# Optimization experiments

Hardware: AMD Instinct MI355X
Metric: run time of the kernel (lower is better)

The kernel has to match this reference:

```python
import jax, jax.numpy as jnp
import numpy as np

H, W, C, B = 64, 64, 512, 16

def _dwconv(x, w, b, k):
    # x: [B,C,H,W]; w: [C,1,k,k] depthwise kernel; b: [C]
    pad = k // 2
    out = jax.lax.conv_general_dilated(
        x, w, window_strides=(1, 1), padding=[(pad, pad), (pad, pad)],
        dimension_numbers=('NCHW', 'OIHW', 'NCHW'), feature_group_count=x.shape[1])
    return out + b[None, :, None, None]

def setup_inputs() -> dict:
    key = jax.random.key(0)
    ks = jax.random.split(key, 7)
    x = jax.random.normal(ks[0], (B, 1 + H * W, C), dtype=jnp.float32)
    def kinit(k, ksize):
        fan_in = ksize * ksize  # groups=C -> in_ch per group = 1
        bound = 1.0 / np.sqrt(fan_in)
        return jax.random.uniform(k, (C, 1, ksize, ksize), jnp.float32, -bound, bound)
    w7 = kinit(ks[1], 7); b7 = jax.random.uniform(ks[2], (C,), jnp.float32, -1/7.0, 1/7.0)
    w5 = kinit(ks[3], 5); b5 = jax.random.uniform(ks[4], (C,), jnp.float32, -1/5.0, 1/5.0)
    w3 = kinit(ks[5], 3); b3 = jax.random.uniform(ks[6], (C,), jnp.float32, -1/3.0, 1/3.0)
    return {'x': x, 'w7': w7, 'b7': b7, 'w5': w5, 'b5': b5, 'w3': w3, 'b3': b3}

def reference(x, w7, b7, w5, b5, w3, b3):
    Bn, N, Cn = x.shape
    cls_token = x[:, 0]          # [B, C]
    feat_token = x[:, 1:]        # [B, H*W, C]
    cnn_feat = feat_token.transpose(0, 2, 1).reshape(Bn, Cn, H, W)
    y = (_dwconv(cnn_feat, w7, b7, 7) + cnn_feat
         + _dwconv(cnn_feat, w5, b5, 5)
         + _dwconv(cnn_feat, w3, b3, 3))
    y = y.reshape(Bn, Cn, H * W).transpose(0, 2, 1)   # [B, HW, C]
    return jnp.concatenate([cls_token[:, None, :], y], axis=1)
```

## Files before the change

kernel.cpp:

```cpp
#include <hip/hip_runtime.h>

#define Hh 64
#define Ww 64
#define Cc 512
#define Bb 16
#define NTOK (1 + Hh * Ww)
#define TW 8
#define TH 2

__global__ void ppeg_prep(const float* __restrict__ w7, const float* __restrict__ b7,
                          const float* __restrict__ w5, const float* __restrict__ b5,
                          const float* __restrict__ w3, const float* __restrict__ b3,
                          const float* __restrict__ x, float* __restrict__ wt,
                          float* __restrict__ beff, float* __restrict__ out) {
    int idx = blockIdx.x * blockDim.x + threadIdx.x;
    if (idx < Cc * 49) {
        int c = idx / 49, t = idx % 49;
        int r = t / 7, s = t % 7;
        float v = w7[idx];
        if (r >= 1 && r <= 5 && s >= 1 && s <= 5) v += w5[c * 25 + (r - 1) * 5 + (s - 1)];
        if (r >= 2 && r <= 4 && s >= 2 && s <= 4) v += w3[c * 9 + (r - 2) * 3 + (s - 2)];
        if (t == 24) v += 1.0f;
        wt[t * Cc + c] = v;
    }
    if (idx < Cc) beff[idx] = b7[idx] + b5[idx] + b3[idx];
    if (idx < Bb * Cc) {
        int b = idx / Cc, c = idx % Cc;
        size_t o = (size_t)b * NTOK * Cc + c;
        out[o] = x[o];
    }
}

__global__ __launch_bounds__(256)
void ppeg_conv(const float* __restrict__ x, const float* __restrict__ wt,
               const float* __restrict__ beff, float* __restrict__ out) {
    const int tx = threadIdx.x;
    const int ty = threadIdx.y;
    const int cb = blockIdx.y * 64;
    const int c  = cb + tx;
    const int b  = blockIdx.z;
    const int sp = blockIdx.x;
    const int hblk  = sp >> 3;
    const int wblk  = sp & 7;
    const int oh0   = hblk * (TH * 4) + ty * TH;
    const int wbase = wblk * TW;

    const float* xb = x + ((size_t)b * NTOK + 1) * Cc + c;

    const float bias = beff[c];
    float acc[TH][TW];
#pragma unroll
    for (int o = 0; o < TH; ++o)
#pragma unroll
        for (int j = 0; j < TW; ++j) acc[o][j] = bias;

    const bool interior = (wblk != 0) && (wblk != 7);

#pragma unroll
    for (int r = 0; r < 7; ++r) {
        float tap[7];
#pragma unroll
        for (int s = 0; s < 7; ++s) tap[s] = wt[(r * 7 + s) * Cc + c];

#pragma unroll
        for (int o = 0; o < TH; ++o) {
            const int ir = oh0 + o + r - 3;
            if (ir < 0 || ir >= Hh) continue;
            const float* xrow = xb + (size_t)ir * Ww * Cc;
            float v[TW + 6];
            if (interior) {
#pragma unroll
                for (int j = 0; j < TW + 6; ++j)
                    v[j] = xrow[(size_t)(wbase - 3 + j) * Cc];
            } else {
#pragma unroll
                for (int j = 0; j < TW + 6; ++j) {
                    const int wc = wbase + j - 3;
                    v[j] = (wc >= 0 && wc < Ww) ? xrow[(size_t)wc * Cc] : 0.0f;
                }
            }
#pragma unroll
            for (int j = 0; j < TW; ++j)
#pragma unroll
                for (int s = 0; s < 7; ++s)
                    acc[o][j] = fmaf(tap[s], v[j + s], acc[o][j]);
        }
    }

#pragma unroll
    for (int o = 0; o < TH; ++o) {
        float* orow = out + ((size_t)b * NTOK + 1 + (size_t)(oh0 + o) * Ww + wbase) * Cc + c;
#pragma unroll
        for (int j = 0; j < TW; ++j) orow[(size_t)j * Cc] = acc[o][j];
    }
}

extern "C" void kernel_launch(void* const* d_in, const int* in_sizes, int n_in,
                              void* d_out, int out_size, void* d_ws, size_t ws_size,
                              hipStream_t stream) {
    const float* x  = (const float*)d_in[0];
    const float* w7 = (const float*)d_in[1];
    const float* b7 = (const float*)d_in[2];
    const float* w5 = (const float*)d_in[3];
    const float* b5 = (const float*)d_in[4];
    const float* w3 = (const float*)d_in[5];
    const float* b3 = (const float*)d_in[6];
    float* out = (float*)d_out;

    float* wt   = (float*)d_ws;
    float* beff = wt + 49 * Cc;

    ppeg_prep<<<(Cc * 49 + 255) / 256, 256, 0, stream>>>(w7, b7, w5, b5, w3, b3,
                                                         x, wt, beff, out);

    dim3 grid((Hh / (TH * 4)) * (Ww / TW), Cc / 64, Bb);
    dim3 block(64, 4);
    ppeg_conv<<<grid, block, 0, stream>>>(x, wt, beff, out);
}
```

Before: 327.0 us.

## Enlarge per-thread row tile and reuse each loaded input row across outputs

Each thread now computes 8 output rows instead of 2. It loads each of the TH+6 input rows once and applies it to every output row that needs it, and all 49 combined taps sit in registers. This cuts redundant global and L2 loads of input rows, from 7 per output row to about 1.75. Output stores become nontemporal and launch bounds request 2 blocks per CU. In exchange, register pressure rises sharply (49 taps plus 64 accumulators plus 14 inputs), which risks spills, and there are fewer blocks in the grid.

Result: faster. 285.6 us (-12.6%).

```diff
diff --git a/kernel.cpp b/kernel.cpp
--- a/kernel.cpp
+++ b/kernel.cpp
@@ -6,7 +6,7 @@
 #define Bb 16
 #define NTOK (1 + Hh * Ww)
 #define TW 8
-#define TH 2
+#define TH 8
 
 __global__ void ppeg_prep(const float* __restrict__ w7, const float* __restrict__ b7,
                           const float* __restrict__ w5, const float* __restrict__ b5,
@@ -31,21 +31,23 @@
     }
 }
 
-__global__ __launch_bounds__(256)
+__global__ __launch_bounds__(256, 2)
 void ppeg_conv(const float* __restrict__ x, const float* __restrict__ wt,
                const float* __restrict__ beff, float* __restrict__ out) {
     const int tx = threadIdx.x;
     const int ty = threadIdx.y;
-    const int cb = blockIdx.y * 64;
-    const int c  = cb + tx;
+    const int c  = blockIdx.y * 64 + tx;
     const int b  = blockIdx.z;
-    const int sp = blockIdx.x;
-    const int hblk  = sp >> 3;
-    const int wblk  = sp & 7;
-    const int oh0   = hblk * (TH * 4) + ty * TH;
+    const int wblk = blockIdx.x & 7;
+    const int hblk = blockIdx.x >> 3;
+    const int oh0   = hblk * 32 + ty * TH;
     const int wbase = wblk * TW;
 
     const float* xb = x + ((size_t)b * NTOK + 1) * Cc + c;
+
+    float tap[49];
+#pragma unroll
+    for (int t = 0; t < 49; ++t) tap[t] = wt[t * Cc + c];
 
     const float bias = beff[c];
     float acc[TH][TW];
@@ -57,16 +59,10 @@
     const bool interior = (wblk != 0) && (wblk != 7);
 
 #pragma unroll
-    for (int r = 0; r < 7; ++r) {
-        float tap[7];
-#pragma unroll
-        for (int s = 0; s < 7; ++s) tap[s] = wt[(r * 7 + s) * Cc + c];
-
-#pragma unroll
-        for (int o = 0; o < TH; ++o) {
-            const int ir = oh0 + o + r - 3;
-            if (ir < 0 || ir >= Hh) continue;
-            const float* xrow = xb + (size_t)ir * Ww * Cc;
+    for (int k = 0; k < TH + 6; ++k) {
+        const int ir = oh0 + k - 3;
+        if (ir >= 0 && ir < Hh) {
+            const float* xrow = xb + (size_t)ir * (Ww * Cc);
             float v[TW + 6];
             if (interior) {
 #pragma unroll
@@ -80,10 +76,17 @@
                 }
             }
 #pragma unroll
-            for (int j = 0; j < TW; ++j)
+            for (int o = 0; o < TH; ++o) {
+                if (o > k || o < k - 6) continue;
+                const int r = k - o;
 #pragma unroll
-                for (int s = 0; s < 7; ++s)
-                    acc[o][j] = fmaf(tap[s], v[j + s], acc[o][j]);
+                for (int s = 0; s < 7; ++s) {
+                    const float tp = tap[r * 7 + s];
+#pragma unroll
+                    for (int j = 0; j < TW; ++j)
+                        acc[o][j] = fmaf(tp, v[j + s], acc[o][j]);
+                }
+            }
         }
     }
 
@@ -91,7 +94,8 @@
     for (int o = 0; o < TH; ++o) {
         float* orow = out + ((size_t)b * NTOK + 1 + (size_t)(oh0 + o) * Ww + wbase) * Cc + c;
 #pragma unroll
-        for (int j = 0; j < TW; ++j) orow[(size_t)j * Cc] = acc[o][j];
+        for (int j = 0; j < TW; ++j)
+            __builtin_nontemporal_store(acc[o][j], &orow[(size_t)j * Cc]);
     }
 }
 
@@ -113,7 +117,7 @@
     ppeg_prep<<<(Cc * 49 + 255) / 256, 256, 0, stream>>>(w7, b7, w5, b5, w3, b3,
                                                          x, wt, beff, out);
 
-    dim3 grid((Hh / (TH * 4)) * (Ww / TW), Cc / 64, Bb);
+    dim3 grid(16, Cc / 64, Bb);
     dim3 block(64, 4);
     ppeg_conv<<<grid, block, 0, stream>>>(x, wt, beff, out);
 }
```
